# Kernel optimization log

Hardware: AMD Instinct MI355X
Metric: run time of the kernel (lower is better)

The kernel has to match this reference:

```python
import jax, jax.numpy as jnp
import numpy as np

RADIUS = 8
NUM = 200
EPS = 1e-8


def _conv2d(x, k, pad_mode):
    # x: [B,1,H,W], k: [kh,kw]; same-size conv with given numpy-style padding mode
    ph, pw = k.shape[0] // 2, k.shape[1] // 2
    xp = jnp.pad(x, ((0, 0), (0, 0), (ph, ph), (pw, pw)), mode=pad_mode)
    return jax.lax.conv_general_dilated(
        xp, k[None, None], (1, 1), 'VALID',
        dimension_numbers=('NCHW', 'OIHW', 'NCHW'))


def _gauss_kernel7():
    xs = np.arange(7, dtype=np.float32) - 3.0
    g = np.exp(-0.5 * xs ** 2)
    g /= g.sum()
    return jnp.asarray(np.outer(g, g))


def get_corners(imgs):
    B, _, H, W = imgs.shape
    # kornia rgb_to_grayscale
    gray = 0.299 * imgs[:, 0:1] + 0.587 * imgs[:, 1:2] + 0.114 * imgs[:, 2:3]
    # kornia CornerGFTT: sobel gradients (normalized), gaussian-smoothed structure tensor, min eigenvalue
    sob = jnp.array([[-1., 0., 1.], [-2., 0., 2.], [-1., 0., 1.]], jnp.float32) / 8.0
    dx = _conv2d(gray, sob, 'edge')
    dy = _conv2d(gray, sob.T, 'edge')
    g = _gauss_kernel7()
    dx2 = _conv2d(dx * dx, g, 'reflect')
    dy2 = _conv2d(dy * dy, g, 'reflect')
    dxy = _conv2d(dx * dy, g, 'reflect')
    tr = dx2 + dy2
    det = dx2 * dy2 - dxy * dxy
    resp = 0.5 * (tr - jnp.sqrt(jnp.abs(tr * tr - 4.0 * det)))  # GFTT score (min eigval)
    # kornia nms2d with 5x5 window: keep local maxima
    mp = jax.lax.reduce_window(resp, -jnp.inf, jax.lax.max,
                               (1, 1, 5, 5), (1, 1, 1, 1),
                               [(0, 0), (0, 0), (2, 2), (2, 2)])
    resp = jnp.where(resp == mp, resp, 0.0)
    # unfold/mask/fold with kernel=stride=RADIUS == per non-overlapping 8x8 block:
    # keep elements equal to the block max and > 0
    r = RADIUS
    blk = resp.reshape(B, 1, H // r, r, W // r, r)
    bmax = blk.max(axis=(3, 5), keepdims=True)
    blk = jnp.where((blk > 0) & (blk == bmax), blk, 0.0)
    corners = blk.reshape(B, H * W)
    # top-200 scatter then binarize
    vals, idx = jax.lax.top_k(corners, NUM)
    out = jnp.zeros_like(corners).at[jnp.arange(B)[:, None], idx].set(vals)
    return (out > 0).astype(imgs.dtype).reshape(B, 1, H, W)


def setup_inputs() -> dict:
    key = jax.random.key(0)
    k1, k2, k3, k4 = jax.random.split(key, 4)
    B, N, D, H, W = 16, 2048, 256, 384, 384
    return {
        'descriptors': jax.random.normal(k1, (B, N, D), jnp.float32),
        'scores': jax.random.uniform(k2, (B, N), jnp.float32),
        'scores_dense': jax.random.normal(k3, (B, 1, H, W), jnp.float32),
        'imgs': jax.random.uniform(k4, (B, 3, H, W), jnp.float32),
    }


def reference(descriptors, scores, scores_dense, imgs):
    corners = get_corners(imgs)
    # all-pairs cosine similarity within each batch: pcos[b,i,j]
    norms = jnp.linalg.norm(descriptors, axis=-1)  # [B,N]
    dots = jnp.einsum('bnd,bmd->bnm', descriptors, descriptors)
    pcos = dots / jnp.maximum(norms[:, :, None] * norms[:, None, :], EPS)
    # BCEWithLogitsLoss(scores_dense, corners), mean reduction
    bce = jnp.mean(jnp.logaddexp(0.0, scores_dense) - scores_dense * corners)
    return bce + jnp.mean(jax.nn.relu(pcos))
```

## Files before the change

kernel.cpp:

```cpp
#include <hip/hip_runtime.h>

#define H 384
#define W 384
#define HWSZ (H * W)
#define NB 16
#define ND 2048
#define DD 256

#define OFF_RESP  256
#define OFF_CVAL  9437440
#define OFF_CPOS  9584896
#define OFF_DESCB 9732352
#define OFF_INV   26509568
#define OFF_PSOFT 26640640
#define OFF_PGEMM 26643200
#define OFF_PCORN 26652160

__device__ __forceinline__ int clampi(int v) { return v < 0 ? 0 : (v > 383 ? 383 : v); }
__device__ __forceinline__ int refl(int v) { return v < 0 ? -v : (v >= 384 ? 766 - v : v); }

__device__ __forceinline__ unsigned f2e4m3(float x) {
  float a = fabsf(x);
  unsigned s = (__float_as_uint(x) >> 31) << 7;
  if (a >= 448.f) return s | 0x7E;
  if (a < 0.015625f) {
    int m = (int)rintf(a * 512.f);
    return s | (unsigned)m;
  }
  unsigned u = __float_as_uint(a);
  u += 0x7FFFF + ((u >> 20) & 1);
  unsigned e = (u >> 23) - 120;
  unsigned m = (u >> 20) & 7;
  return s | (e << 3) | m;
}

typedef float f32x4 __attribute__((ext_vector_type(4)));

__device__ __forceinline__ void load_lds16(const void* g, void* l) {
  __builtin_amdgcn_global_load_lds((const __attribute__((address_space(1))) void*)g,
                                   (__attribute__((address_space(3))) void*)l, 16, 0, 0);
}

__global__ __launch_bounds__(256) void stage1_kernel(const float* __restrict__ imgs,
                                                     float* __restrict__ resp,
                                                     const float* __restrict__ desc,
                                                     unsigned char* __restrict__ descF8,
                                                     float* __restrict__ invn) {
  __shared__ float gl[40][41];
  __shared__ float p0[38][39], p1[38][39], p2[38][39];
  __shared__ float t0[38][33], t1[38][33], t2[38][33];

  if (blockIdx.x >= 2304) {
    int wave = threadIdx.x >> 6, lane = threadIdx.x & 63;
    int row = (blockIdx.x - 2304) * 4 + wave;
    const float4* src = (const float4*)(desc + (size_t)row * DD);
    float4 v = src[lane];
    unsigned pk = f2e4m3(v.x) | (f2e4m3(v.y) << 8) | (f2e4m3(v.z) << 16) | (f2e4m3(v.w) << 24);
    ((unsigned*)(descF8 + (size_t)row * DD))[lane] = pk;
    float ss = v.x * v.x + v.y * v.y + v.z * v.z + v.w * v.w;
    for (int off = 32; off; off >>= 1) ss += __shfl_down(ss, off, 64);
    if (lane == 0) invn[row] = 1.f / fmaxf(sqrtf(ss), 1e-4f);
    return;
  }

  const float GW[7] = {0.0044330482f, 0.0540055826f, 0.2420362294f, 0.3990502160f,
                       0.2420362294f, 0.0540055826f, 0.0044330482f};
  int bid = blockIdx.x;
  int b = bid / 144;
  int t = bid % 144;
  int Y0 = (t / 12) * 32, X0 = (t % 12) * 32;
  const float* ib = imgs + (size_t)b * 3 * HWSZ;

  for (int i = threadIdx.x; i < 1600; i += 256) {
    int r = i / 40, c = i % 40;
    int gy = clampi(Y0 - 4 + r), gx = clampi(X0 - 4 + c);
    const float* p = ib + gy * W + gx;
    gl[r][c] = 0.299f * p[0] + 0.587f * p[HWSZ] + 0.114f * p[2 * HWSZ];
  }
  __syncthreads();

  for (int i = threadIdx.x; i < 1444; i += 256) {
    int r = i / 38, c = i % 38;
    int py = refl(Y0 - 3 + r), px = refl(X0 - 3 + c);
    int ym = clampi(py - 1) - (Y0 - 4), y0 = py - (Y0 - 4), yp = clampi(py + 1) - (Y0 - 4);
    int xm = clampi(px - 1) - (X0 - 4), x0 = px - (X0 - 4), xp = clampi(px + 1) - (X0 - 4);
    float a = gl[ym][xm], bb = gl[ym][x0], cc = gl[ym][xp];
    float d = gl[y0][xm], e = gl[y0][xp];
    float f = gl[yp][xm], g = gl[yp][x0], h = gl[yp][xp];
    float dx = 0.125f * ((cc - a) + 2.f * (e - d) + (h - f));
    float dy = 0.125f * ((f - a) + 2.f * (g - bb) + (h - cc));
    p0[r][c] = dx * dx;
    p1[r][c] = dy * dy;
    p2[r][c] = dx * dy;
  }
  __syncthreads();

  for (int i = threadIdx.x; i < 1216; i += 256) {
    int r = i / 32, c = i % 32;
    float s0 = 0.f, s1 = 0.f, s2 = 0.f;
#pragma unroll
    for (int j = 0; j < 7; j++) {
      s0 += GW[j] * p0[r][c + j];
      s1 += GW[j] * p1[r][c + j];
      s2 += GW[j] * p2[r][c + j];
    }
    t0[r][c] = s0; t1[r][c] = s1; t2[r][c] = s2;
  }
  __syncthreads();

  for (int i = threadIdx.x; i < 1024; i += 256) {
    int r = i / 32, c = i % 32;
    float s0 = 0.f, s1 = 0.f, s2 = 0.f;
#pragma unroll
    for (int j = 0; j < 7; j++) {
      s0 += GW[j] * t0[r + j][c];
      s1 += GW[j] * t1[r + j][c];
      s2 += GW[j] * t2[r + j][c];
    }
    float tr = s0 + s1;
    float det = s0 * s1 - s2 * s2;
    float disc = tr * tr - 4.f * det;
    float rv = 0.5f * (tr - sqrtf(fabsf(disc)));
    resp[(size_t)b * HWSZ + (Y0 + r) * W + (X0 + c)] = rv;
  }
}

__global__ __launch_bounds__(256) void stage2_kernel(const float* __restrict__ resp,
                                                     float* __restrict__ cval,
                                                     unsigned* __restrict__ cpos,
                                                     const float4* __restrict__ sd4,
                                                     float* __restrict__ psoft) {
  __shared__ float rl[68][69];
  __shared__ float nl[64][65];
  __shared__ float r4[4];

  if (blockIdx.x >= 576) {
    int sb = blockIdx.x - 576;
    float s = 0.f;
    int base = sb * 256 + threadIdx.x;
#pragma unroll
    for (int it = 0; it < 4; it++) {
      float4 v = sd4[base + it * 147456];
      s += fmaxf(v.x, 0.f) + log1pf(expf(-fabsf(v.x))) +
           fmaxf(v.y, 0.f) + log1pf(expf(-fabsf(v.y))) +
           fmaxf(v.z, 0.f) + log1pf(expf(-fabsf(v.z))) +
           fmaxf(v.w, 0.f) + log1pf(expf(-fabsf(v.w)));
    }
    for (int off = 32; off; off >>= 1) s += __shfl_down(s, off, 64);
    if ((threadIdx.x & 63) == 0) r4[threadIdx.x >> 6] = s;
    __syncthreads();
    if (threadIdx.x == 0) psoft[sb] = r4[0] + r4[1] + r4[2] + r4[3];
    return;
  }

  int bid = blockIdx.x;
  int b = bid / 36;
  int t = bid % 36;
  int Y0 = (t / 6) * 64, X0 = (t % 6) * 64;
  const float* rb = resp + (size_t)b * HWSZ;

  for (int i = threadIdx.x; i < 68 * 68; i += 256) {
    int r = i / 68, c = i % 68;
    int gy = Y0 - 2 + r, gx = X0 - 2 + c;
    float v = -INFINITY;
    if (gy >= 0 && gy < H && gx >= 0 && gx < W) v = rb[gy * W + gx];
    rl[r][c] = v;
  }
  __syncthreads();

  for (int i = threadIdx.x; i < 4096; i += 256) {
    int r = i / 64, c = i % 64;
    float m = -INFINITY;
#pragma unroll
    for (int dr = 0; dr < 5; dr++)
#pragma unroll
      for (int dc = 0; dc < 5; dc++) m = fmaxf(m, rl[r + dr][c + dc]);
    float v = rl[r + 2][c + 2];
    nl[r][c] = (v == m) ? v : 0.f;
  }
  __syncthreads();

  if (threadIdx.x < 64) {
    int bi = threadIdx.x / 8, bj = threadIdx.x % 8;
    float bv = 0.f;
    unsigned bp = 0;
    for (int rr = 0; rr < 8; rr++)
      for (int cc = 0; cc < 8; cc++) {
        float v = nl[bi * 8 + rr][bj * 8 + cc];
        if (v > bv) { bv = v; bp = (unsigned)((Y0 + bi * 8 + rr) * W + (X0 + bj * 8 + cc)); }
      }
    int ci = b * 2304 + (Y0 / 8 + bi) * 48 + (X0 / 8 + bj);
    cval[ci] = bv;
    cpos[ci] = bp;
  }
}

__global__ __launch_bounds__(256) void stage3_kernel(const float* __restrict__ cval,
                                                     const unsigned* __restrict__ cpos,
                                                     const float* __restrict__ sd,
                                                     float* __restrict__ pcorn,
                                                     const unsigned char* __restrict__ descF8,
                                                     const float* __restrict__ invn,
                                                     float* __restrict__ pgemm) {
  __shared__ char lA[128 * 128];
  __shared__ char lB[128 * 128];
  __shared__ float r4[4];
  __shared__ int hist[256];
  __shared__ int pick[2];
  __shared__ unsigned eqpos[256];
  __shared__ int eqcnt;
  __shared__ int ri[4];

  if (blockIdx.x < 16) {
    int b = blockIdx.x;
    int t = threadIdx.x;
    int lane = t & 63;

    unsigned bits[9], pos[9];
#pragma unroll
    for (int q = 0; q < 9; q++) {
      int i = t + q * 256;
      unsigned vb = 0, p = 0;
      if (i < 2304) {
        float v = cval[b * 2304 + i];
        if (v > 0.f) { vb = __float_as_uint(v); p = cpos[b * 2304 + i]; }
      }
      bits[q] = vb; pos[q] = p;
    }

    int P = 0;
#pragma unroll
    for (int q = 0; q < 9; q++) P += (bits[q] != 0u);
    for (int off = 32; off; off >>= 1) P += __shfl_down(P, off, 64);
    if (lane == 0) ri[t >> 6] = P;
    __syncthreads();
    int Ptot = ri[0] + ri[1] + ri[2] + ri[3];
    if (Ptot == 0) { if (t == 0) pcorn[b] = 0.f; return; }
    int K = Ptot < 200 ? Ptot : 200;

    unsigned prefix = 0;
    int krem = K;
    for (int shift = 24; shift >= 0; shift -= 8) {
      hist[t] = 0;
      __syncthreads();
#pragma unroll
      for (int q = 0; q < 9; q++) {
        if (bits[q] != 0u &&
            (shift == 24 || (bits[q] >> (shift + 8)) == (prefix >> (shift + 8))))
          atomicAdd(&hist[(bits[q] >> shift) & 0xFF], 1);
      }
      __syncthreads();
      if (t < 64) {
        int h0 = hist[4 * t], h1 = hist[4 * t + 1], h2 = hist[4 * t + 2], h3 = hist[4 * t + 3];
        int tot = h0 + h1 + h2 + h3;
        int acc = tot;
        for (int d = 1; d < 64; d <<= 1) {
          int o = __shfl_down(acc, d, 64);
          if (t + d < 64) acc += o;
        }
        int excl = acc - tot;
        int G3 = excl, G2 = excl + h3, G1 = excl + h3 + h2, G0 = excl + h3 + h2 + h1;
        if (G0 < krem && G0 + h0 >= krem) { pick[0] = 4 * t;     pick[1] = G0; }
        if (G1 < krem && G1 + h1 >= krem) { pick[0] = 4 * t + 1; pick[1] = G1; }
        if (G2 < krem && G2 + h2 >= krem) { pick[0] = 4 * t + 2; pick[1] = G2; }
        if (G3 < krem && G3 + h3 >= krem) { pick[0] = 4 * t + 3; pick[1] = G3; }
      }
      __syncthreads();
      prefix |= ((unsigned)pick[0]) << shift;
      krem -= pick[1];
      __syncthreads();
    }

    if (t == 0) eqcnt = 0;
    __syncthreads();
    float s = 0.f;
#pragma unroll
    for (int q = 0; q < 9; q++) {
      if (bits[q] > prefix) s += sd[(size_t)b * HWSZ + pos[q]];
      else if (bits[q] != 0u && bits[q] == prefix) {
        int idx = atomicAdd(&eqcnt, 1);
        if (idx < 256) eqpos[idx] = pos[q];
      }
    }
    __syncthreads();
    int m = eqcnt;
    if (m <= krem) {
      if (t < m) s += sd[(size_t)b * HWSZ + eqpos[t]];
    } else {
      int mm = m < 256 ? m : 256;
      if (t < mm) {
        unsigned p = eqpos[t];
        int rank = 0;
        for (int u = 0; u < mm; u++) rank += (eqpos[u] < p);
        if (rank < krem) s += sd[(size_t)b * HWSZ + p];
      }
    }
    for (int off = 32; off; off >>= 1) s += __shfl_down(s, off, 64);
    if (lane == 0) r4[t >> 6] = s;
    __syncthreads();
    if (t == 0) pcorn[b] = r4[0] + r4[1] + r4[2] + r4[3];
    return;
  }

  int bx = blockIdx.x - 16;
  int batch = bx / 136;
  int rem = bx % 136;
  int ti = 0, rowlen = 16;
  while (rem >= rowlen) { rem -= rowlen; rowlen--; ti++; }
  int tj = ti + rem;

  const unsigned char* Ab = descF8 + (size_t)batch * ND * DD;
  const float* inv = invn + batch * ND;
  int I0 = ti * 128, J0 = tj * 128;

  int tid = threadIdx.x;
  int wave = tid >> 6, lane = tid & 63;
  int rm = lane & 15, kq = lane >> 4;
  int wr = wave >> 1, wc = wave & 1;
  int lrow = lane >> 3;
  int lcolb = ((lane & 7) ^ lrow) << 4;
  int cx = rm & 7;

  f32x4 accf[4][4];
#pragma unroll
  for (int m = 0; m < 4; m++)
#pragma unroll
    for (int n = 0; n < 4; n++) accf[m][n] = (f32x4){0.f, 0.f, 0.f, 0.f};

  for (int k0 = 0; k0 < DD; k0 += 128) {
#pragma unroll
    for (int q = 0; q < 4; q++) {
      int chunk = wave * 4 + q;
      load_lds16(Ab + (size_t)(I0 + chunk * 8 + lrow) * DD + k0 + lcolb, lA + chunk * 1024);
      load_lds16(Ab + (size_t)(J0 + chunk * 8 + lrow) * DD + k0 + lcolb, lB + chunk * 1024);
    }
    __syncthreads();
#pragma unroll
    for (int kk = 0; kk < 128; kk += 32) {
      long af[4], bfr[4];
      int koff = kk + kq * 8;
      int pcol = ((((koff >> 4) ^ cx) << 4) | (koff & 8));
#pragma unroll
      for (int m = 0; m < 4; m++)
        af[m] = *reinterpret_cast<const long*>(lA + (wr * 64 + m * 16 + rm) * 128 + pcol);
#pragma unroll
      for (int n = 0; n < 4; n++)
        bfr[n] = *reinterpret_cast<const long*>(lB + (wc * 64 + n * 16 + rm) * 128 + pcol);
#pragma unroll
      for (int m = 0; m < 4; m++)
#pragma unroll
        for (int n = 0; n < 4; n++)
          accf[m][n] = __builtin_amdgcn_mfma_f32_16x16x32_fp8_fp8(af[m], bfr[n], accf[m][n], 0, 0, 0);
    }
    __syncthreads();
  }

  float wgt = (ti == tj) ? 1.f : 2.f;
  float invC[4];
#pragma unroll
  for (int n = 0; n < 4; n++) invC[n] = inv[J0 + wc * 64 + n * 16 + rm];
  float psum = 0.f;
#pragma unroll
  for (int m = 0; m < 4; m++) {
#pragma unroll
    for (int r = 0; r < 4; r++) {
      float invR = inv[I0 + wr * 64 + m * 16 + kq * 4 + r];
#pragma unroll
      for (int n = 0; n < 4; n++) psum += fmaxf(accf[m][n][r] * invR * invC[n], 0.f);
    }
  }
  psum *= wgt;
  for (int off = 32; off; off >>= 1) psum += __shfl_down(psum, off, 64);
  if (lane == 0) r4[wave] = psum;
  __syncthreads();
  if (tid == 0) pgemm[bx] = r4[0] + r4[1] + r4[2] + r4[3];
}

__global__ __launch_bounds__(256) void finalize_kernel(const float* __restrict__ psoft,
                                                       const float* __restrict__ pcorn,
                                                       const float* __restrict__ pgemm,
                                                       float* __restrict__ out) {
  __shared__ float r4[4];
  float bce = 0.f;
  for (int i = threadIdx.x; i < 576; i += 256) bce += psoft[i];
  if (threadIdx.x < 16) bce -= pcorn[threadIdx.x];
  float g = 0.f;
  for (int i = threadIdx.x; i < 2176; i += 256) g += pgemm[i];
  float t = bce * (1.f / 2359296.f) + g * (1.f / 67108864.f);
  for (int off = 32; off; off >>= 1) t += __shfl_down(t, off, 64);
  if ((threadIdx.x & 63) == 0) r4[threadIdx.x >> 6] = t;
  __syncthreads();
  if (threadIdx.x == 0) out[0] = r4[0] + r4[1] + r4[2] + r4[3];
}

extern "C" void kernel_launch(void* const* d_in, const int* in_sizes, int n_in,
                              void* d_out, int out_size, void* d_ws, size_t ws_size,
                              hipStream_t stream) {
  (void)in_sizes; (void)n_in; (void)out_size; (void)ws_size;
  const float* desc = (const float*)d_in[0];
  const float* sd = (const float*)d_in[2];
  const float* imgs = (const float*)d_in[3];
  float* out = (float*)d_out;

  char* w = (char*)d_ws;
  float* resp = (float*)(w + OFF_RESP);
  float* cval = (float*)(w + OFF_CVAL);
  unsigned* cpos = (unsigned*)(w + OFF_CPOS);
  unsigned char* descF8 = (unsigned char*)(w + OFF_DESCB);
  float* invn = (float*)(w + OFF_INV);
  float* psoft = (float*)(w + OFF_PSOFT);
  float* pgemm = (float*)(w + OFF_PGEMM);
  float* pcorn = (float*)(w + OFF_PCORN);

  stage1_kernel<<<10496, 256, 0, stream>>>(imgs, resp, desc, descF8, invn);
  stage2_kernel<<<1152, 256, 0, stream>>>(resp, cval, cpos, (const float4*)sd, psoft);
  stage3_kernel<<<2192, 256, 0, stream>>>(cval, cpos, sd, pcorn, descF8, invn, pgemm);
  finalize_kernel<<<1, 256, 0, stream>>>(psoft, pcorn, pgemm, out);
}
```

Before: 160.0 us.

## Rebalance stage work across kernels and register-block the interior structure-tensor convolutions

Moves the softplus reduction into stage1, runs the NMS/block-max work alongside the FP8 similarity GEMM in stage2 using dynamic shared memory, and splits the per-batch top-k selection into its own small kernel. Interior 32x32 tiles get a register-blocked path that computes 4 outputs per thread for the Sobel, horizontal and vertical Gaussian passes, which cuts redundant LDS reads and index arithmetic. The aim is to reduce the serial tail, where 16 top-k blocks previously shared a launch with the GEMM, and to make better use of the GPU. The cost is an extra kernel launch and larger shared memory per block in stage2, which may lower occupancy for the GEMM.

```diff
diff --git a/kernel.cpp b/kernel.cpp
--- a/kernel.cpp
+++ b/kernel.cpp
@@ -45,10 +45,32 @@
                                                      float* __restrict__ resp,
                                                      const float* __restrict__ desc,
                                                      unsigned char* __restrict__ descF8,
-                                                     float* __restrict__ invn) {
+                                                     float* __restrict__ invn,
+                                                     const float4* __restrict__ sd4,
+                                                     float* __restrict__ psoft) {
   __shared__ float gl[40][41];
   __shared__ float p0[38][39], p1[38][39], p2[38][39];
   __shared__ float t0[38][33], t1[38][33], t2[38][33];
+  __shared__ float r4s[4];
+
+  if (blockIdx.x >= 10496) {
+    int sb = blockIdx.x - 10496;
+    float s = 0.f;
+    int base = sb * 256 + threadIdx.x;
+#pragma unroll
+    for (int it = 0; it < 4; it++) {
+      float4 v = sd4[base + it * 147456];
+      s += fmaxf(v.x, 0.f) + log1pf(expf(-fabsf(v.x))) +
+           fmaxf(v.y, 0.f) + log1pf(expf(-fabsf(v.y))) +
+           fmaxf(v.z, 0.f) + log1pf(expf(-fabsf(v.z))) +
+           fmaxf(v.w, 0.f) + log1pf(expf(-fabsf(v.w)));
+    }
+    for (int off = 32; off; off >>= 1) s += __shfl_down(s, off, 64);
+    if ((threadIdx.x & 63) == 0) r4s[threadIdx.x >> 6] = s;
+    __syncthreads();
+    if (threadIdx.x == 0) psoft[sb] = r4s[0] + r4s[1] + r4s[2] + r4s[3];
+    return;
+  }
 
   if (blockIdx.x >= 2304) {
     int wave = threadIdx.x >> 6, lane = threadIdx.x & 63;
@@ -78,6 +100,79 @@
     gl[r][c] = 0.299f * p[0] + 0.587f * p[HWSZ] + 0.114f * p[2 * HWSZ];
   }
   __syncthreads();
+
+  bool interior = (X0 >= 32 && X0 <= 320 && Y0 >= 32 && Y0 <= 320);
+
+  if (interior) {
+    for (int g = threadIdx.x; g < 380; g += 256) {
+      int r = g % 38, c0 = (g / 38) * 4;
+      float w0[6], w1[6], w2[6];
+#pragma unroll
+      for (int dc = 0; dc < 6; dc++) {
+        int cc = c0 + dc; if (cc > 39) cc = 39;
+        w0[dc] = gl[r][cc]; w1[dc] = gl[r + 1][cc]; w2[dc] = gl[r + 2][cc];
+      }
+#pragma unroll
+      for (int k = 0; k < 4; k++) {
+        int cc = c0 + k;
+        if (cc < 38) {
+          float a = w0[k], bb = w0[k + 1], cv = w0[k + 2];
+          float d = w1[k], e = w1[k + 2];
+          float f = w2[k], gg = w2[k + 1], h = w2[k + 2];
+          float dx = 0.125f * ((cv - a) + 2.f * (e - d) + (h - f));
+          float dy = 0.125f * ((f - a) + 2.f * (gg - bb) + (h - cv));
+          p0[r][cc] = dx * dx;
+          p1[r][cc] = dy * dy;
+          p2[r][cc] = dx * dy;
+        }
+      }
+    }
+    __syncthreads();
+    for (int g = threadIdx.x; g < 304; g += 256) {
+      int r = g >> 3, c0 = (g & 7) * 4;
+      float a0[10], a1[10], a2[10];
+#pragma unroll
+      for (int dc = 0; dc < 10; dc++) {
+        a0[dc] = p0[r][c0 + dc]; a1[dc] = p1[r][c0 + dc]; a2[dc] = p2[r][c0 + dc];
+      }
+#pragma unroll
+      for (int k = 0; k < 4; k++) {
+        float s0 = 0.f, s1 = 0.f, s2 = 0.f;
+#pragma unroll
+        for (int j = 0; j < 7; j++) {
+          s0 += GW[j] * a0[k + j];
+          s1 += GW[j] * a1[k + j];
+          s2 += GW[j] * a2[k + j];
+        }
+        t0[r][c0 + k] = s0; t1[r][c0 + k] = s1; t2[r][c0 + k] = s2;
+      }
+    }
+    __syncthreads();
+    {
+      int rg = (threadIdx.x >> 5) * 4, c = threadIdx.x & 31;
+      float a0[10], a1[10], a2[10];
+#pragma unroll
+      for (int dr = 0; dr < 10; dr++) {
+        a0[dr] = t0[rg + dr][c]; a1[dr] = t1[rg + dr][c]; a2[dr] = t2[rg + dr][c];
+      }
+#pragma unroll
+      for (int k = 0; k < 4; k++) {
+        float s0 = 0.f, s1 = 0.f, s2 = 0.f;
+#pragma unroll
+        for (int j = 0; j < 7; j++) {
+          s0 += GW[j] * a0[k + j];
+          s1 += GW[j] * a1[k + j];
+          s2 += GW[j] * a2[k + j];
+        }
+        float tr = s0 + s1;
+        float det = s0 * s1 - s2 * s2;
+        float disc = tr * tr - 4.f * det;
+        float rv = 0.5f * (tr - sqrtf(fabsf(disc)));
+        resp[(size_t)b * HWSZ + (Y0 + rg + k) * W + (X0 + c)] = rv;
+      }
+    }
+    return;
+  }
 
   for (int i = threadIdx.x; i < 1444; i += 256) {
     int r = i / 38, c = i % 38;
@@ -125,184 +220,65 @@
   }
 }
 
-__global__ __launch_bounds__(256) void stage2_kernel(const float* __restrict__ resp,
+__global__ __launch_bounds__(256) void stage2_kernel(const unsigned char* __restrict__ descF8,
+                                                     const float* __restrict__ invn,
+                                                     float* __restrict__ pgemm,
+                                                     const float* __restrict__ resp,
                                                      float* __restrict__ cval,
-                                                     unsigned* __restrict__ cpos,
-                                                     const float4* __restrict__ sd4,
-                                                     float* __restrict__ psoft) {
-  __shared__ float rl[68][69];
-  __shared__ float nl[64][65];
-  __shared__ float r4[4];
-
-  if (blockIdx.x >= 576) {
-    int sb = blockIdx.x - 576;
-    float s = 0.f;
-    int base = sb * 256 + threadIdx.x;
-#pragma unroll
-    for (int it = 0; it < 4; it++) {
-      float4 v = sd4[base + it * 147456];
-      s += fmaxf(v.x, 0.f) + log1pf(expf(-fabsf(v.x))) +
-           fmaxf(v.y, 0.f) + log1pf(expf(-fabsf(v.y))) +
-           fmaxf(v.z, 0.f) + log1pf(expf(-fabsf(v.z))) +
-           fmaxf(v.w, 0.f) + log1pf(expf(-fabsf(v.w)));
-    }
-    for (int off = 32; off; off >>= 1) s += __shfl_down(s, off, 64);
-    if ((threadIdx.x & 63) == 0) r4[threadIdx.x >> 6] = s;
-    __syncthreads();
-    if (threadIdx.x == 0) psoft[sb] = r4[0] + r4[1] + r4[2] + r4[3];
+                                                     unsigned* __restrict__ cpos) {
+  extern __shared__ char smem2[];
+
+  if (blockIdx.x >= 2176) {
+    float (*rl)[69] = (float(*)[69])smem2;
+    float (*nl)[65] = (float(*)[65])(smem2 + 68 * 69 * 4);
+    int bid = blockIdx.x - 2176;
+    int b = bid / 36;
+    int t = bid % 36;
+    int Y0 = (t / 6) * 64, X0 = (t % 6) * 64;
+    const float* rb = resp + (size_t)b * HWSZ;
+
+    for (int i = threadIdx.x; i < 68 * 68; i += 256) {
+      int r = i / 68, c = i % 68;
+      int gy = Y0 - 2 + r, gx = X0 - 2 + c;
+      float v = -INFINITY;
+      if (gy >= 0 && gy < H && gx >= 0 && gx < W) v = rb[gy * W + gx];
+      rl[r][c] = v;
+    }
+    __syncthreads();
+
+    for (int i = threadIdx.x; i < 4096; i += 256) {
+      int r = i / 64, c = i % 64;
+      float m = -INFINITY;
+#pragma unroll
+      for (int dr = 0; dr < 5; dr++)
+#pragma unroll
+        for (int dc = 0; dc < 5; dc++) m = fmaxf(m, rl[r + dr][c + dc]);
+      float v = rl[r + 2][c + 2];
+      nl[r][c] = (v == m) ? v : 0.f;
+    }
+    __syncthreads();
+
+    if (threadIdx.x < 64) {
+      int bi = threadIdx.x / 8, bj = threadIdx.x % 8;
+      float bv = 0.f;
+      unsigned bp = 0;
+      for (int rr = 0; rr < 8; rr++)
+        for (int cc = 0; cc < 8; cc++) {
+          float v = nl[bi * 8 + rr][bj * 8 + cc];
+          if (v > bv) { bv = v; bp = (unsigned)((Y0 + bi * 8 + rr) * W + (X0 + bj * 8 + cc)); }
+        }
+      int ci = b * 2304 + (Y0 / 8 + bi) * 48 + (X0 / 8 + bj);
+      cval[ci] = bv;
+      cpos[ci] = bp;
+    }
     return;
   }
 
-  int bid = blockIdx.x;
-  int b = bid / 36;
-  int t = bid % 36;
-  int Y0 = (t / 6) * 64, X0 = (t % 6) * 64;
-  const float* rb = resp + (size_t)b * HWSZ;
-
-  for (int i = threadIdx.x; i < 68 * 68; i += 256) {
-    int r = i / 68, c = i % 68;
-    int gy = Y0 - 2 + r, gx = X0 - 2 + c;
-    float v = -INFINITY;
-    if (gy >= 0 && gy < H && gx >= 0 && gx < W) v = rb[gy * W + gx];
-    rl[r][c] = v;
-  }
-  __syncthreads();
-
-  for (int i = threadIdx.x; i < 4096; i += 256) {
-    int r = i / 64, c = i % 64;
-    float m = -INFINITY;
-#pragma unroll
-    for (int dr = 0; dr < 5; dr++)
-#pragma unroll
-      for (int dc = 0; dc < 5; dc++) m = fmaxf(m, rl[r + dr][c + dc]);
-    float v = rl[r + 2][c + 2];
-    nl[r][c] = (v == m) ? v : 0.f;
-  }
-  __syncthreads();
-
-  if (threadIdx.x < 64) {
-    int bi = threadIdx.x / 8, bj = threadIdx.x % 8;
-    float bv = 0.f;
-    unsigned bp = 0;
-    for (int rr = 0; rr < 8; rr++)
-      for (int cc = 0; cc < 8; cc++) {
-        float v = nl[bi * 8 + rr][bj * 8 + cc];
-        if (v > bv) { bv = v; bp = (unsigned)((Y0 + bi * 8 + rr) * W + (X0 + bj * 8 + cc)); }
-      }
-    int ci = b * 2304 + (Y0 / 8 + bi) * 48 + (X0 / 8 + bj);
-    cval[ci] = bv;
-    cpos[ci] = bp;
-  }
-}
-
-__global__ __launch_bounds__(256) void stage3_kernel(const float* __restrict__ cval,
-                                                     const unsigned* __restrict__ cpos,
-                                                     const float* __restrict__ sd,
-                                                     float* __restrict__ pcorn,
-                                                     const unsigned char* __restrict__ descF8,
-                                                     const float* __restrict__ invn,
-                                                     float* __restrict__ pgemm) {
-  __shared__ char lA[128 * 128];
-  __shared__ char lB[128 * 128];
-  __shared__ float r4[4];
-  __shared__ int hist[256];
-  __shared__ int pick[2];
-  __shared__ unsigned eqpos[256];
-  __shared__ int eqcnt;
-  __shared__ int ri[4];
-
-  if (blockIdx.x < 16) {
-    int b = blockIdx.x;
-    int t = threadIdx.x;
-    int lane = t & 63;
-
-    unsigned bits[9], pos[9];
-#pragma unroll
-    for (int q = 0; q < 9; q++) {
-      int i = t + q * 256;
-      unsigned vb = 0, p = 0;
-      if (i < 2304) {
-        float v = cval[b * 2304 + i];
-        if (v > 0.f) { vb = __float_as_uint(v); p = cpos[b * 2304 + i]; }
-      }
-      bits[q] = vb; pos[q] = p;
-    }
-
-    int P = 0;
-#pragma unroll
-    for (int q = 0; q < 9; q++) P += (bits[q] != 0u);
-    for (int off = 32; off; off >>= 1) P += __shfl_down(P, off, 64);
-    if (lane == 0) ri[t >> 6] = P;
-    __syncthreads();
-    int Ptot = ri[0] + ri[1] + ri[2] + ri[3];
-    if (Ptot == 0) { if (t == 0) pcorn[b] = 0.f; return; }
-    int K = Ptot < 200 ? Ptot : 200;
-
-    unsigned prefix = 0;
-    int krem = K;
-    for (int shift = 24; shift >= 0; shift -= 8) {
-      hist[t] = 0;
-      __syncthreads();
-#pragma unroll
-      for (int q = 0; q < 9; q++) {
-        if (bits[q] != 0u &&
-            (shift == 24 || (bits[q] >> (shift + 8)) == (prefix >> (shift + 8))))
-          atomicAdd(&hist[(bits[q] >> shift) & 0xFF], 1);
-      }
-      __syncthreads();
-      if (t < 64) {
-        int h0 = hist[4 * t], h1 = hist[4 * t + 1], h2 = hist[4 * t + 2], h3 = hist[4 * t + 3];
-        int tot = h0 + h1 + h2 + h3;
-        int acc = tot;
-        for (int d = 1; d < 64; d <<= 1) {
-          int o = __shfl_down(acc, d, 64);
-          if (t + d < 64) acc += o;
-        }
-        int excl = acc - tot;
-        int G3 = excl, G2 = excl + h3, G1 = excl + h3 + h2, G0 = excl + h3 + h2 + h1;
-        if (G0 < krem && G0 + h0 >= krem) { pick[0] = 4 * t;     pick[1] = G0; }
-        if (G1 < krem && G1 + h1 >= krem) { pick[0] = 4 * t + 1; pick[1] = G1; }
-        if (G2 < krem && G2 + h2 >= krem) { pick[0] = 4 * t + 2; pick[1] = G2; }
-        if (G3 < krem && G3 + h3 >= krem) { pick[0] = 4 * t + 3; pick[1] = G3; }
-      }
-      __syncthreads();
-      prefix |= ((unsigned)pick[0]) << shift;
-      krem -= pick[1];
-      __syncthreads();
-    }
-
-    if (t == 0) eqcnt = 0;
-    __syncthreads();
-    float s = 0.f;
-#pragma unroll
-    for (int q = 0; q < 9; q++) {
-      if (bits[q] > prefix) s += sd[(size_t)b * HWSZ + pos[q]];
-      else if (bits[q] != 0u && bits[q] == prefix) {
-        int idx = atomicAdd(&eqcnt, 1);
-        if (idx < 256) eqpos[idx] = pos[q];
-      }
-    }
-    __syncthreads();
-    int m = eqcnt;
-    if (m <= krem) {
-      if (t < m) s += sd[(size_t)b * HWSZ + eqpos[t]];
-    } else {
-      int mm = m < 256 ? m : 256;
-      if (t < mm) {
-        unsigned p = eqpos[t];
-        int rank = 0;
-        for (int u = 0; u < mm; u++) rank += (eqpos[u] < p);
-        if (rank < krem) s += sd[(size_t)b * HWSZ + p];
-      }
-    }
-    for (int off = 32; off; off >>= 1) s += __shfl_down(s, off, 64);
-    if (lane == 0) r4[t >> 6] = s;
-    __syncthreads();
-    if (t == 0) pcorn[b] = r4[0] + r4[1] + r4[2] + r4[3];
-    return;
-  }
-
-  int bx = blockIdx.x - 16;
+  char* lA = smem2;
+  char* lB = smem2 + 16384;
+  float* r4 = (float*)(smem2 + 32768);
+
+  int bx = blockIdx.x;
   int batch = bx / 136;
   int rem = bx % 136;
   int ti = 0, rowlen = 16;
@@ -374,6 +350,106 @@
   if (lane == 0) r4[wave] = psum;
   __syncthreads();
   if (tid == 0) pgemm[bx] = r4[0] + r4[1] + r4[2] + r4[3];
+}
+
+__global__ __launch_bounds__(256) void topk_kernel(const float* __restrict__ cval,
+                                                   const unsigned* __restrict__ cpos,
+                                                   const float* __restrict__ sd,
+                                                   float* __restrict__ pcorn) {
+  __shared__ int hist[256];
+  __shared__ int pick[2];
+  __shared__ unsigned eqpos[256];
+  __shared__ int eqcnt;
+  __shared__ float rf[4];
+  __shared__ int ri[4];
+
+  int b = blockIdx.x;
+  int t = threadIdx.x;
+  int lane = t & 63;
+
+  unsigned bits[9], pos[9];
+#pragma unroll
+  for (int q = 0; q < 9; q++) {
+    int i = t + q * 256;
+    unsigned vb = 0, p = 0;
+    if (i < 2304) {
+      float v = cval[b * 2304 + i];
+      if (v > 0.f) { vb = __float_as_uint(v); p = cpos[b * 2304 + i]; }
+    }
+    bits[q] = vb; pos[q] = p;
+  }
+
+  int P = 0;
+#pragma unroll
+  for (int q = 0; q < 9; q++) P += (bits[q] != 0u);
+  for (int off = 32; off; off >>= 1) P += __shfl_down(P, off, 64);
+  if (lane == 0) ri[t >> 6] = P;
+  __syncthreads();
+  int Ptot = ri[0] + ri[1] + ri[2] + ri[3];
+  if (Ptot == 0) { if (t == 0) pcorn[b] = 0.f; return; }
+  int K = Ptot < 200 ? Ptot : 200;
+
+  unsigned prefix = 0;
+  int krem = K;
+  for (int shift = 24; shift >= 0; shift -= 8) {
+    hist[t] = 0;
+    __syncthreads();
+#pragma unroll
+    for (int q = 0; q < 9; q++) {
+      if (bits[q] != 0u &&
+          (shift == 24 || (bits[q] >> (shift + 8)) == (prefix >> (shift + 8))))
+        atomicAdd(&hist[(bits[q] >> shift) & 0xFF], 1);
+    }
+    __syncthreads();
+    if (t < 64) {
+      int h0 = hist[4 * t], h1 = hist[4 * t + 1], h2 = hist[4 * t + 2], h3 = hist[4 * t + 3];
+      int tot = h0 + h1 + h2 + h3;
+      int acc = tot;
+      for (int d = 1; d < 64; d <<= 1) {
+        int o = __shfl_down(acc, d, 64);
+        if (t + d < 64) acc += o;
+      }
+      int excl = acc - tot;
+      int G3 = excl, G2 = excl + h3, G1 = excl + h3 + h2, G0 = excl + h3 + h2 + h1;
+      if (G0 < krem && G0 + h0 >= krem) { pick[0] = 4 * t;     pick[1] = G0; }
+      if (G1 < krem && G1 + h1 >= krem) { pick[0] = 4 * t + 1; pick[1] = G1; }
+      if (G2 < krem && G2 + h2 >= krem) { pick[0] = 4 * t + 2; pick[1] = G2; }
+      if (G3 < krem && G3 + h3 >= krem) { pick[0] = 4 * t + 3; pick[1] = G3; }
+    }
+    __syncthreads();
+    prefix |= ((unsigned)pick[0]) << shift;
+    krem -= pick[1];
+    __syncthreads();
+  }
+
+  if (t == 0) eqcnt = 0;
+  __syncthreads();
+  float s = 0.f;
+#pragma unroll
+  for (int q = 0; q < 9; q++) {
+    if (bits[q] > prefix) s += sd[(size_t)b * HWSZ + pos[q]];
+    else if (bits[q] != 0u && bits[q] == prefix) {
+      int idx = atomicAdd(&eqcnt, 1);
+      if (idx < 256) eqpos[idx] = pos[q];
+    }
+  }
+  __syncthreads();
+  int m = eqcnt;
+  if (m <= krem) {
+    if (t < m) s += sd[(size_t)b * HWSZ + eqpos[t]];
+  } else {
+    int mm = m < 256 ? m : 256;
+    if (t < mm) {
+      unsigned p = eqpos[t];
+      int rank = 0;
+      for (int u = 0; u < mm; u++) rank += (eqpos[u] < p);
+      if (rank < krem) s += sd[(size_t)b * HWSZ + p];
+    }
+  }
+  for (int off = 32; off; off >>= 1) s += __shfl_down(s, off, 64);
+  if (lane == 0) rf[t >> 6] = s;
+  __syncthreads();
+  if (t == 0) pcorn[b] = rf[0] + rf[1] + rf[2] + rf[3];
 }
 
 __global__ __launch_bounds__(256) void finalize_kernel(const float* __restrict__ psoft,
@@ -412,8 +488,9 @@
   float* pgemm = (float*)(w + OFF_PGEMM);
   float* pcorn = (float*)(w + OFF_PCORN);
 
-  stage1_kernel<<<10496, 256, 0, stream>>>(imgs, resp, desc, descF8, invn);
-  stage2_kernel<<<1152, 256, 0, stream>>>(resp, cval, cpos, (const float4*)sd, psoft);
-  stage3_kernel<<<2192, 256, 0, stream>>>(cval, cpos, sd, pcorn, descF8, invn, pgemm);
+  stage1_kernel<<<11072, 256, 0, stream>>>(imgs, resp, desc, descF8, invn,
+                                           (const float4*)sd, psoft);
+  stage2_kernel<<<2752, 256, 35456, stream>>>(descF8, invn, pgemm, resp, cval, cpos);
+  topk_kernel<<<16, 256, 0, stream>>>(cval, cpos, sd, pcorn);
   finalize_kernel<<<1, 256, 0, stream>>>(psoft, pcorn, pgemm, out);
 }
```

Result: slower. 177.0 us (+10.6%).
